# Performance work log

Measured on AMD Instinct MI355X. Metric: run time of the kernel, lower is better.

## Reference

```python
import jax, jax.numpy as jnp
import numpy as np

N, E, G, L, H, DIN = 50000, 800000, 500, 4, 64, 128
EPS = 1e-5


def _gcn(x, W, b, src, dst, n):
    h = x @ W
    loop = jnp.arange(n)
    s = jnp.concatenate([src, loop])
    d = jnp.concatenate([dst, loop])
    deg = jax.ops.segment_sum(jnp.ones(s.shape[0], x.dtype), d, num_segments=n)
    dinv = jax.lax.rsqrt(jnp.maximum(deg, 1.0))  # deg >= 1 due to self loops
    norm = (dinv[s] * dinv[d])[:, None]
    return jax.ops.segment_sum(h[s] * norm, d, num_segments=n) + b


def _g2(x, W, b, src, dst, n, p=2.0):
    # G2 gradient gate: tau = tanh(scatter_mean_over_src(|X_src - X_dst|^p))
    Xc = jax.nn.relu(_gcn(x, W, b, src, dst, n))
    diff = jnp.abs(Xc[src] - Xc[dst]) ** p  # [E, H]
    s = jax.ops.segment_sum(diff, src, num_segments=n)
    cnt = jax.ops.segment_sum(jnp.ones(src.shape[0], x.dtype), src, num_segments=n)
    return jnp.tanh(s / jnp.maximum(cnt, 1.0)[:, None])


def _bn(x, g, b):
    # BatchNorm1d with batch statistics (training-mode normalization)
    m = x.mean(0)
    v = x.var(0)
    return (x - m) * jax.lax.rsqrt(v + EPS) * g + b


def setup_inputs() -> dict:
    key = jax.random.key(0)
    ks = jax.random.split(key, 24)
    sc_in = 1.0 / np.sqrt(DIN)
    sc_h = 1.0 / np.sqrt(H)
    inp = {
        "x": jax.random.normal(ks[0], (N, DIN), jnp.float32),
        "edge_index": jax.random.randint(ks[1], (2, E), 0, N),
        "batch": jnp.sort(jax.random.randint(ks[2], (N,), 0, G)),
        "preW": jax.random.normal(ks[3], (DIN, H), jnp.float32) * sc_in,
        "preb": jnp.zeros((H,), jnp.float32),
        "convW": jax.random.normal(ks[4], (L, H, H), jnp.float32) * sc_h,
        "convb": jnp.zeros((L, H), jnp.float32),
        "ggW": jax.random.normal(ks[5], (L, H, H), jnp.float32) * sc_h,
        "ggb": jnp.zeros((L, H), jnp.float32),
        "lin1W": jax.random.normal(ks[6], (H, H), jnp.float32) * sc_h,
        "lin1b": jnp.zeros((H,), jnp.float32),
        "lin2W": jax.random.normal(ks[7], (H, H), jnp.float32) * sc_h,
        "lin2b": jnp.zeros((H,), jnp.float32),
        "lin3W": jax.random.normal(ks[8], (H, H), jnp.float32) * sc_h,
        "lin3b": jnp.zeros((H,), jnp.float32),
        "lin4W": jax.random.normal(ks[9], (H, 1), jnp.float32) * sc_h,
        "lin4b": jnp.zeros((1,), jnp.float32),
        "bn_g": jnp.ones((H,), jnp.float32),
        "bn_b": jnp.zeros((H,), jnp.float32),
    }
    return inp


def reference(x, edge_index, batch, preW, preb, convW, convb, ggW, ggb,
              lin1W, lin1b, lin2W, lin2b, lin3W, lin3b, lin4W, lin4b,
              bn_g, bn_b):
    src, dst = edge_index[0], edge_index[1]
    # prelinear (dropout disabled / eval)
    x = jax.nn.relu(x @ preW + preb)
    for l in range(L):
        x_ = jax.nn.relu(_gcn(x, convW[l], convb[l], src, dst, N))
        tau = _g2(x, ggW[l], ggb[l], src, dst, N)
        x = (1.0 - tau) * x + tau * x_
    # readout: global add pool per graph -> [G, H]
    h = jax.ops.segment_sum(x, batch, num_segments=G)
    out = jax.nn.relu(_bn(h @ lin1W + lin1b, bn_g, bn_b))
    out = jax.nn.relu(_bn(out @ lin2W + lin2b, bn_g, bn_b))
    out = jax.nn.relu(_bn(out @ lin3W + lin3b, bn_g, bn_b))
    out = out @ lin4W + lin4b  # [G, 1]
    energy = 0.5 * jnp.sum((x[src] - x[dst]) ** 2)  # dirichlet energy of final x
    return (out, out, energy)
```

## Files before the change

kernel.cpp:

```cpp
#include <hip/hip_runtime.h>
#include <hip/hip_bf16.h>


#define N_NODES 50000
#define N_EDGES 800000
#define N_GRAPH 500
#define N_LAYERS 4
#define HDIM 64
#define DDIN 128
#define BN_EPS 1e-5f
#define NEPART 256


__global__ __launch_bounds__(256) void k_degrees(const int* __restrict__ ei,
                                                 int* __restrict__ deg_in,
                                                 int* __restrict__ deg_out) {
  int e = blockIdx.x * 256 + threadIdx.x;
  if (e >= N_EDGES) return;
  int s = ei[e], d = ei[N_EDGES + e];
  atomicAdd(&deg_out[s], 1);
  atomicAdd(&deg_in[d], 1);
}

__global__ __launch_bounds__(1024) void k_scan(const int* __restrict__ a0, int* __restrict__ o0,
                                               int* __restrict__ c0,
                                               const int* __restrict__ a1, int* __restrict__ o1,
                                               int* __restrict__ c1) {
  __shared__ int sh[1024];
  const int T = 1024, C = 8;
  for (int pass = 0; pass < 2; ++pass) {
    const int* in = pass ? a1 : a0;
    int* out = pass ? o1 : o0;
    int* cur = pass ? c1 : c0;
    int carry = 0;
    for (int base = 0; base < N_NODES; base += T * C) {
      int idx0 = base + threadIdx.x * C;
      int v[C];
      int s = 0;
#pragma unroll
      for (int j = 0; j < C; ++j) {
        int ii = idx0 + j;
        v[j] = (ii < N_NODES) ? in[ii] : 0;
        s += v[j];
      }
      sh[threadIdx.x] = s;
      __syncthreads();
      for (int off = 1; off < T; off <<= 1) {
        int t = (threadIdx.x >= off) ? sh[threadIdx.x - off] : 0;
        __syncthreads();
        if (threadIdx.x >= off) sh[threadIdx.x] += t;
        __syncthreads();
      }
      int incl = sh[threadIdx.x];
      int excl = incl - s;
      int run = carry + excl;
#pragma unroll
      for (int j = 0; j < C; ++j) {
        int ii = idx0 + j;
        if (ii < N_NODES) {
          out[ii] = run;
          cur[ii] = run;
        }
        run += v[j];
      }
      int total = sh[T - 1];
      __syncthreads();
      carry += total;
    }
    if (threadIdx.x == 0) out[N_NODES] = carry;
    __syncthreads();
  }
}

__global__ __launch_bounds__(256) void k_fill(const int* __restrict__ ei,
                                              int* __restrict__ cur_dst,
                                              int* __restrict__ cur_src,
                                              int* __restrict__ csr_dst,
                                              int* __restrict__ csr_src) {
  int e = blockIdx.x * 256 + threadIdx.x;
  if (e >= N_EDGES) return;
  int s = ei[e], d = ei[N_EDGES + e];
  int p = atomicAdd(&cur_dst[d], 1);
  csr_dst[p] = s;
  int q = atomicAdd(&cur_src[s], 1);
  csr_src[q] = d;
}

__global__ __launch_bounds__(256) void k_dinv(const int* __restrict__ deg_in,
                                              float* __restrict__ dinv) {
  int i = blockIdx.x * 256 + threadIdx.x;
  if (i >= N_NODES) return;
  dinv[i] = rsqrtf((float)(deg_in[i] + 1));
}


__global__ __launch_bounds__(256) void k_prelin(const float* __restrict__ x0,
                                                const float* __restrict__ W,
                                                const float* __restrict__ b,
                                                float* __restrict__ x) {
  __shared__ float Ws[DDIN * HDIM];
  for (int t = threadIdx.x; t < DDIN * HDIM; t += 256) Ws[t] = W[t];
  __syncthreads();
  int wave = threadIdx.x >> 6, lane = threadIdx.x & 63;
  float bias = b[lane];
  int stride = gridDim.x * 4;
  for (int i = blockIdx.x * 4 + wave; i < N_NODES; i += stride) {
    const float* xr = x0 + (size_t)i * DDIN;
    float xl0 = xr[lane], xl1 = xr[64 + lane];
    float acc = bias;
#pragma unroll
    for (int k = 0; k < 64; ++k) acc = fmaf(__shfl(xl0, k), Ws[k * 64 + lane], acc);
#pragma unroll
    for (int k = 0; k < 64; ++k) acc = fmaf(__shfl(xl1, k), Ws[(64 + k) * 64 + lane], acc);
    x[(size_t)i * HDIM + lane] = fmaxf(acc, 0.f);
  }
}

__global__ __launch_bounds__(256) void k_gemm2(const float* __restrict__ agg,
                                               const float* __restrict__ W1,
                                               const float* __restrict__ W2,
                                               const float* __restrict__ b1,
                                               const float* __restrict__ b2,
                                               float* __restrict__ x_,
                                               float* __restrict__ Xc) {
  __shared__ float W1s[HDIM * HDIM], W2s[HDIM * HDIM];
  for (int t = threadIdx.x; t < HDIM * HDIM; t += 256) {
    W1s[t] = W1[t];
    W2s[t] = W2[t];
  }
  __syncthreads();
  int wave = threadIdx.x >> 6, lane = threadIdx.x & 63;
  float bb1 = b1[lane], bb2 = b2[lane];
  int stride = gridDim.x * 4;
  for (int i = blockIdx.x * 4 + wave; i < N_NODES; i += stride) {
    float xl = agg[(size_t)i * HDIM + lane];
    float a1 = 0.f, a2 = 0.f;
#pragma unroll
    for (int k = 0; k < 64; ++k) {
      float xv = __shfl(xl, k);
      a1 = fmaf(xv, W1s[k * 64 + lane], a1);
      a2 = fmaf(xv, W2s[k * 64 + lane], a2);
    }
    x_[(size_t)i * HDIM + lane] = fmaxf(a1 + bb1, 0.f);
    Xc[(size_t)i * HDIM + lane] = fmaxf(a2 + bb2, 0.f);
  }
}


__global__ __launch_bounds__(256) void k_agg(const float* __restrict__ x,
                                             const int* __restrict__ rp,
                                             const int* __restrict__ csr,
                                             const float* __restrict__ dinv,
                                             float* __restrict__ agg) {
  int i = (blockIdx.x * 256 + threadIdx.x) >> 6;
  int lane = threadIdx.x & 63;
  if (i >= N_NODES) return;
  int e0 = rp[i], e1 = rp[i + 1];
  float di = dinv[i];
  size_t li = (size_t)i * HDIM + lane;
  float a0 = x[li] * di, a1 = 0.f, a2 = 0.f, a3 = 0.f;
  for (int base = e0; base < e1; base += 64) {
    int m = e1 - base;
    if (m > 64) m = 64;
    int idx = csr[base + (lane < m ? lane : 0)];
    float dv = dinv[idx];
    int k = 0;
    for (; k + 8 <= m; k += 8) {
      int s0 = __shfl(idx, k), s1 = __shfl(idx, k + 1), s2 = __shfl(idx, k + 2),
          s3 = __shfl(idx, k + 3), s4 = __shfl(idx, k + 4), s5 = __shfl(idx, k + 5),
          s6 = __shfl(idx, k + 6), s7 = __shfl(idx, k + 7);
      float w0 = __shfl(dv, k), w1 = __shfl(dv, k + 1), w2 = __shfl(dv, k + 2),
            w3 = __shfl(dv, k + 3), w4 = __shfl(dv, k + 4), w5 = __shfl(dv, k + 5),
            w6 = __shfl(dv, k + 6), w7 = __shfl(dv, k + 7);
      float v0 = x[(size_t)s0 * HDIM + lane], v1 = x[(size_t)s1 * HDIM + lane];
      float v2 = x[(size_t)s2 * HDIM + lane], v3 = x[(size_t)s3 * HDIM + lane];
      float v4 = x[(size_t)s4 * HDIM + lane], v5 = x[(size_t)s5 * HDIM + lane];
      float v6 = x[(size_t)s6 * HDIM + lane], v7 = x[(size_t)s7 * HDIM + lane];
      a0 = fmaf(v0, w0, a0);
      a1 = fmaf(v1, w1, a1);
      a2 = fmaf(v2, w2, a2);
      a3 = fmaf(v3, w3, a3);
      a0 = fmaf(v4, w4, a0);
      a1 = fmaf(v5, w5, a1);
      a2 = fmaf(v6, w6, a2);
      a3 = fmaf(v7, w7, a3);
    }
    for (; k < m; ++k) {
      int s = __shfl(idx, k);
      float w = __shfl(dv, k);
      a0 = fmaf(x[(size_t)s * HDIM + lane], w, a0);
    }
  }
  agg[li] = (a0 + a1 + a2 + a3) * di;
}

__global__ __launch_bounds__(256) void k_gate(const float* __restrict__ Xc,
                                              const float* __restrict__ x_,
                                              const int* __restrict__ rp,
                                              const int* __restrict__ csr,
                                              float* __restrict__ x) {
  int i = (blockIdx.x * 256 + threadIdx.x) >> 6;
  int lane = threadIdx.x & 63;
  if (i >= N_NODES) return;
  int e0 = rp[i], e1 = rp[i + 1];
  float xi = Xc[(size_t)i * HDIM + lane];
  float a0 = 0.f, a1 = 0.f, a2 = 0.f, a3 = 0.f;
  for (int base = e0; base < e1; base += 64) {
    int m = e1 - base;
    if (m > 64) m = 64;
    int idx = csr[base + (lane < m ? lane : 0)];
    int k = 0;
    for (; k + 8 <= m; k += 8) {
      int s0 = __shfl(idx, k), s1 = __shfl(idx, k + 1), s2 = __shfl(idx, k + 2),
          s3 = __shfl(idx, k + 3), s4 = __shfl(idx, k + 4), s5 = __shfl(idx, k + 5),
          s6 = __shfl(idx, k + 6), s7 = __shfl(idx, k + 7);
      float v0 = Xc[(size_t)s0 * HDIM + lane], v1 = Xc[(size_t)s1 * HDIM + lane];
      float v2 = Xc[(size_t)s2 * HDIM + lane], v3 = Xc[(size_t)s3 * HDIM + lane];
      float v4 = Xc[(size_t)s4 * HDIM + lane], v5 = Xc[(size_t)s5 * HDIM + lane];
      float v6 = Xc[(size_t)s6 * HDIM + lane], v7 = Xc[(size_t)s7 * HDIM + lane];
      float t0 = xi - v0, t1 = xi - v1, t2 = xi - v2, t3 = xi - v3;
      float t4 = xi - v4, t5 = xi - v5, t6 = xi - v6, t7 = xi - v7;
      a0 = fmaf(t0, t0, a0);
      a1 = fmaf(t1, t1, a1);
      a2 = fmaf(t2, t2, a2);
      a3 = fmaf(t3, t3, a3);
      a0 = fmaf(t4, t4, a0);
      a1 = fmaf(t5, t5, a1);
      a2 = fmaf(t6, t6, a2);
      a3 = fmaf(t7, t7, a3);
    }
    for (; k < m; ++k) {
      int d = __shfl(idx, k);
      float t = xi - Xc[(size_t)d * HDIM + lane];
      a0 = fmaf(t, t, a0);
    }
  }
  int cnt = e1 - e0;
  float tau = tanhf((a0 + a1 + a2 + a3) / (float)(cnt > 0 ? cnt : 1));
  size_t idx = (size_t)i * HDIM + lane;
  x[idx] = (1.f - tau) * x[idx] + tau * x_[idx];
}

__global__ __launch_bounds__(256) void k_epool(const float* __restrict__ x,
                                               const int* __restrict__ rp,
                                               const int* __restrict__ csr,
                                               const int* __restrict__ batch,
                                               float* __restrict__ hpool,
                                               float* __restrict__ epart) {
  int i = (blockIdx.x * 256 + threadIdx.x) >> 6;
  int lane = threadIdx.x & 63;
  if (i >= N_NODES) return;
  float xi = x[(size_t)i * HDIM + lane];
  int e0 = rp[i], e1 = rp[i + 1];
  float a0 = 0.f, a1 = 0.f, a2 = 0.f, a3 = 0.f;
  for (int base = e0; base < e1; base += 64) {
    int m = e1 - base;
    if (m > 64) m = 64;
    int idx = csr[base + (lane < m ? lane : 0)];
    int k = 0;
    for (; k + 8 <= m; k += 8) {
      int s0 = __shfl(idx, k), s1 = __shfl(idx, k + 1), s2 = __shfl(idx, k + 2),
          s3 = __shfl(idx, k + 3), s4 = __shfl(idx, k + 4), s5 = __shfl(idx, k + 5),
          s6 = __shfl(idx, k + 6), s7 = __shfl(idx, k + 7);
      float v0 = x[(size_t)s0 * HDIM + lane], v1 = x[(size_t)s1 * HDIM + lane];
      float v2 = x[(size_t)s2 * HDIM + lane], v3 = x[(size_t)s3 * HDIM + lane];
      float v4 = x[(size_t)s4 * HDIM + lane], v5 = x[(size_t)s5 * HDIM + lane];
      float v6 = x[(size_t)s6 * HDIM + lane], v7 = x[(size_t)s7 * HDIM + lane];
      float t0 = xi - v0, t1 = xi - v1, t2 = xi - v2, t3 = xi - v3;
      float t4 = xi - v4, t5 = xi - v5, t6 = xi - v6, t7 = xi - v7;
      a0 = fmaf(t0, t0, a0);
      a1 = fmaf(t1, t1, a1);
      a2 = fmaf(t2, t2, a2);
      a3 = fmaf(t3, t3, a3);
      a0 = fmaf(t4, t4, a0);
      a1 = fmaf(t5, t5, a1);
      a2 = fmaf(t6, t6, a2);
      a3 = fmaf(t7, t7, a3);
    }
    for (; k < m; ++k) {
      int d = __shfl(idx, k);
      float t = xi - x[(size_t)d * HDIM + lane];
      a0 = fmaf(t, t, a0);
    }
  }
  int g = batch[i];
  atomicAdd(&hpool[g * HDIM + lane], xi);
  float acc = a0 + a1 + a2 + a3;
  acc += __shfl_down(acc, 32);
  acc += __shfl_down(acc, 16);
  acc += __shfl_down(acc, 8);
  acc += __shfl_down(acc, 4);
  acc += __shfl_down(acc, 2);
  acc += __shfl_down(acc, 1);
  if (lane == 0) atomicAdd(&epart[i & (NEPART - 1)], acc);
}

__global__ __launch_bounds__(256) void k_esum(const float* __restrict__ epart,
                                              float* __restrict__ out_e) {
  __shared__ float sh[NEPART];
  int t = threadIdx.x;
  sh[t] = epart[t];
  __syncthreads();
  for (int off = NEPART / 2; off > 0; off >>= 1) {
    if (t < off) sh[t] += sh[t + off];
    __syncthreads();
  }
  if (t == 0) out_e[0] = 0.5f * sh[0];
}


__global__ __launch_bounds__(64) void k_mlp(const float* __restrict__ Hin,
                                            const float* __restrict__ W,
                                            const float* __restrict__ b,
                                            float* __restrict__ Z) {
  int r = blockIdx.x, c = threadIdx.x;
  float xl = Hin[r * HDIM + c];
  float acc = b[c];
#pragma unroll
  for (int k = 0; k < 64; ++k) acc = fmaf(__shfl(xl, k), W[k * HDIM + c], acc);
  Z[r * HDIM + c] = acc;
}

__global__ __launch_bounds__(256) void k_bn(float* __restrict__ Z,
                                            const float* __restrict__ g,
                                            const float* __restrict__ b) {
  int c = blockIdx.x;
  int tid = threadIdx.x;
  __shared__ float red[256];
  float v0 = (tid < N_GRAPH) ? Z[tid * HDIM + c] : 0.f;
  float v1 = (tid + 256 < N_GRAPH) ? Z[(tid + 256) * HDIM + c] : 0.f;
  red[tid] = v0 + v1;
  __syncthreads();
  for (int off = 128; off > 0; off >>= 1) {
    if (tid < off) red[tid] += red[tid + off];
    __syncthreads();
  }
  float mean = red[0] / (float)N_GRAPH;
  __syncthreads();
  float d0 = (tid < N_GRAPH) ? v0 - mean : 0.f;
  float d1 = (tid + 256 < N_GRAPH) ? v1 - mean : 0.f;
  red[tid] = d0 * d0 + d1 * d1;
  __syncthreads();
  for (int off = 128; off > 0; off >>= 1) {
    if (tid < off) red[tid] += red[tid + off];
    __syncthreads();
  }
  float var = red[0] / (float)N_GRAPH;
  float scale = rsqrtf(var + BN_EPS) * g[c];
  float bias = b[c];
  if (tid < N_GRAPH) Z[tid * HDIM + c] = fmaxf(fmaf(d0, scale, bias), 0.f);
  if (tid + 256 < N_GRAPH) Z[(tid + 256) * HDIM + c] = fmaxf(fmaf(d1, scale, bias), 0.f);
}

__global__ __launch_bounds__(256) void k_final(const float* __restrict__ H,
                                               const float* __restrict__ w,
                                               const float* __restrict__ b,
                                               float* __restrict__ out) {
  int r = blockIdx.x * 256 + threadIdx.x;
  if (r >= N_GRAPH) return;
  float acc = b[0];
#pragma unroll
  for (int k = 0; k < 64; ++k) acc = fmaf(H[r * HDIM + k], w[k], acc);
  out[r] = acc;
  out[N_GRAPH + r] = acc;
}


extern "C" void kernel_launch(void* const* d_in, const int* in_sizes, int n_in,
                              void* d_out, int out_size, void* d_ws, size_t ws_size,
                              hipStream_t stream) {
  (void)in_sizes; (void)n_in; (void)out_size; (void)ws_size;
  const float* x0    = (const float*)d_in[0];
  const int*   ei    = (const int*)d_in[1];
  const int*   batch = (const int*)d_in[2];
  const float* preW  = (const float*)d_in[3];
  const float* preb  = (const float*)d_in[4];
  const float* convW = (const float*)d_in[5];
  const float* convb = (const float*)d_in[6];
  const float* ggW   = (const float*)d_in[7];
  const float* ggb   = (const float*)d_in[8];
  const float* lin1W = (const float*)d_in[9];
  const float* lin1b = (const float*)d_in[10];
  const float* lin2W = (const float*)d_in[11];
  const float* lin2b = (const float*)d_in[12];
  const float* lin3W = (const float*)d_in[13];
  const float* lin3b = (const float*)d_in[14];
  const float* lin4W = (const float*)d_in[15];
  const float* lin4b = (const float*)d_in[16];
  const float* bng   = (const float*)d_in[17];
  const float* bnb   = (const float*)d_in[18];
  float* out = (float*)d_out;

  char* ws = (char*)d_ws;
  size_t off = 0;
  auto alloc = [&](size_t bytes) -> void* {
    off = (off + 255) & ~(size_t)255;
    void* p = ws + off;
    off += bytes;
    return p;
  };
  int* deg_in   = (int*)alloc(2ull * N_NODES * 4);
  int* deg_out  = deg_in + N_NODES;
  int* rp_dst   = (int*)alloc((N_NODES + 1) * 4);
  int* rp_src   = (int*)alloc((N_NODES + 1) * 4);
  int* cur_dst  = (int*)alloc((N_NODES + 1) * 4);
  int* cur_src  = (int*)alloc((N_NODES + 1) * 4);
  int* csr_dst  = (int*)alloc((size_t)N_EDGES * 4);
  int* csr_src  = (int*)alloc((size_t)N_EDGES * 4);
  float* dinv   = (float*)alloc(N_NODES * 4);
  float* x      = (float*)alloc((size_t)N_NODES * HDIM * 4);
  float* aggb   = (float*)alloc((size_t)N_NODES * HDIM * 4);
  float* x_     = (float*)alloc((size_t)N_NODES * HDIM * 4);
  float* Xc     = (float*)alloc((size_t)N_NODES * HDIM * 4);
  float* hpool  = (float*)alloc(N_GRAPH * HDIM * 4);
  float* epart  = (float*)alloc(NEPART * 4);
  float* mlpA   = (float*)alloc(N_GRAPH * HDIM * 4);
  float* mlpB   = (float*)alloc(N_GRAPH * HDIM * 4);

  hipMemsetAsync(deg_in, 0, 2ull * N_NODES * 4, stream);
  hipMemsetAsync(hpool, 0, N_GRAPH * HDIM * 4, stream);
  hipMemsetAsync(epart, 0, NEPART * 4, stream);

  k_degrees<<<(N_EDGES + 255) / 256, 256, 0, stream>>>(ei, deg_in, deg_out);
  k_scan<<<1, 1024, 0, stream>>>(deg_in, rp_dst, cur_dst, deg_out, rp_src, cur_src);
  k_fill<<<(N_EDGES + 255) / 256, 256, 0, stream>>>(ei, cur_dst, cur_src, csr_dst, csr_src);
  k_dinv<<<(N_NODES + 255) / 256, 256, 0, stream>>>(deg_in, dinv);

  k_prelin<<<512, 256, 0, stream>>>(x0, preW, preb, x);

  const int gnode = (N_NODES + 3) / 4;
  for (int l = 0; l < N_LAYERS; ++l) {
    k_agg<<<gnode, 256, 0, stream>>>(x, rp_dst, csr_dst, dinv, aggb);
    k_gemm2<<<1024, 256, 0, stream>>>(aggb, convW + l * HDIM * HDIM, ggW + l * HDIM * HDIM,
                                      convb + l * HDIM, ggb + l * HDIM, x_, Xc);
    k_gate<<<gnode, 256, 0, stream>>>(Xc, x_, rp_src, csr_src, x);
  }

  k_epool<<<gnode, 256, 0, stream>>>(x, rp_src, csr_src, batch, hpool, epart);
  k_esum<<<1, NEPART, 0, stream>>>(epart, out + 2 * N_GRAPH);

  k_mlp<<<N_GRAPH, 64, 0, stream>>>(hpool, lin1W, lin1b, mlpA);
  k_bn<<<HDIM, 256, 0, stream>>>(mlpA, bng, bnb);
  k_mlp<<<N_GRAPH, 64, 0, stream>>>(mlpA, lin2W, lin2b, mlpB);
  k_bn<<<HDIM, 256, 0, stream>>>(mlpB, bng, bnb);
  k_mlp<<<N_GRAPH, 64, 0, stream>>>(mlpB, lin3W, lin3b, mlpA);
  k_bn<<<HDIM, 256, 0, stream>>>(mlpA, bng, bnb);
  k_final<<<(N_GRAPH + 255) / 256, 256, 0, stream>>>(mlpA, lin4W, lin4b, out);
}
```

Before: 1.073 ms.

## Parallelize CSR prefix scan across blocks and fuse aggregation into dual GEMM

Replaces the single-block serial scan with a three-phase multi-block scan (block scans, block-offset scan, offset add) that also computes dinv, removing one launch. Fuses the GCN neighbor aggregation into the dual 64x64 GEMM kernel so the aggregated features stay in registers instead of round-tripping through a global buffer each layer. The fused kernel uses a persistent grid of 1024 blocks with 32KB shared memory for weights, which may lower occupancy and latency hiding for the gather-heavy aggregation.

```diff
diff --git a/kernel.cpp b/kernel.cpp
--- a/kernel.cpp
+++ b/kernel.cpp
@@ -10,6 +10,8 @@
 #define DDIN 128
 #define BN_EPS 1e-5f
 #define NEPART 256
+#define SC_CHUNK 2048
+#define SC_NBLK ((N_NODES + SC_CHUNK - 1) / SC_CHUNK)
 
 
 __global__ __launch_bounds__(256) void k_degrees(const int* __restrict__ ei,
@@ -22,53 +24,83 @@
   atomicAdd(&deg_in[d], 1);
 }
 
-__global__ __launch_bounds__(1024) void k_scan(const int* __restrict__ a0, int* __restrict__ o0,
-                                               int* __restrict__ c0,
-                                               const int* __restrict__ a1, int* __restrict__ o1,
-                                               int* __restrict__ c1) {
-  __shared__ int sh[1024];
-  const int T = 1024, C = 8;
-  for (int pass = 0; pass < 2; ++pass) {
-    const int* in = pass ? a1 : a0;
-    int* out = pass ? o1 : o0;
-    int* cur = pass ? c1 : c0;
-    int carry = 0;
-    for (int base = 0; base < N_NODES; base += T * C) {
-      int idx0 = base + threadIdx.x * C;
-      int v[C];
-      int s = 0;
-#pragma unroll
-      for (int j = 0; j < C; ++j) {
-        int ii = idx0 + j;
-        v[j] = (ii < N_NODES) ? in[ii] : 0;
-        s += v[j];
-      }
-      sh[threadIdx.x] = s;
-      __syncthreads();
-      for (int off = 1; off < T; off <<= 1) {
-        int t = (threadIdx.x >= off) ? sh[threadIdx.x - off] : 0;
-        __syncthreads();
-        if (threadIdx.x >= off) sh[threadIdx.x] += t;
-        __syncthreads();
-      }
-      int incl = sh[threadIdx.x];
-      int excl = incl - s;
-      int run = carry + excl;
-#pragma unroll
-      for (int j = 0; j < C; ++j) {
-        int ii = idx0 + j;
-        if (ii < N_NODES) {
-          out[ii] = run;
-          cur[ii] = run;
-        }
-        run += v[j];
-      }
-      int total = sh[T - 1];
-      __syncthreads();
-      carry += total;
-    }
-    if (threadIdx.x == 0) out[N_NODES] = carry;
+__global__ __launch_bounds__(256) void k_scan1(const int* __restrict__ deg_in,
+                                               const int* __restrict__ deg_out,
+                                               int* __restrict__ rp_dst,
+                                               int* __restrict__ rp_src,
+                                               int* __restrict__ bsum) {
+  int arr = blockIdx.y;
+  const int* in = arr ? deg_out : deg_in;
+  int* out = arr ? rp_src : rp_dst;
+  int base = blockIdx.x * SC_CHUNK + threadIdx.x * 8;
+  int v[8];
+  int s = 0;
+#pragma unroll
+  for (int j = 0; j < 8; ++j) {
+    int ii = base + j;
+    v[j] = (ii < N_NODES) ? in[ii] : 0;
+    s += v[j];
+  }
+  __shared__ int sh[256];
+  sh[threadIdx.x] = s;
+  __syncthreads();
+  for (int off = 1; off < 256; off <<= 1) {
+    int t = (threadIdx.x >= off) ? sh[threadIdx.x - off] : 0;
     __syncthreads();
+    sh[threadIdx.x] += t;
+    __syncthreads();
+  }
+  int run = sh[threadIdx.x] - s;
+#pragma unroll
+  for (int j = 0; j < 8; ++j) {
+    int ii = base + j;
+    if (ii < N_NODES) out[ii] = run;
+    run += v[j];
+  }
+  if (threadIdx.x == 255) bsum[arr * SC_NBLK + blockIdx.x] = sh[255];
+}
+
+__global__ __launch_bounds__(64) void k_scan2(const int* __restrict__ bsum,
+                                              int* __restrict__ boff,
+                                              int* __restrict__ rp_dst,
+                                              int* __restrict__ rp_src) {
+  int lane = threadIdx.x;
+  for (int a = 0; a < 2; ++a) {
+    int v = (lane < SC_NBLK) ? bsum[a * SC_NBLK + lane] : 0;
+    int incl = v;
+    for (int off = 1; off < 64; off <<= 1) {
+      int t = __shfl_up(incl, off);
+      if (lane >= off) incl += t;
+    }
+    if (lane < SC_NBLK) boff[a * SC_NBLK + lane] = incl - v;
+  }
+  if (lane == 0) {
+    rp_dst[N_NODES] = N_EDGES;
+    rp_src[N_NODES] = N_EDGES;
+  }
+}
+
+__global__ __launch_bounds__(256) void k_scan3(const int* __restrict__ boff,
+                                               int* __restrict__ rp_dst,
+                                               int* __restrict__ rp_src,
+                                               int* __restrict__ cur_dst,
+                                               int* __restrict__ cur_src,
+                                               const int* __restrict__ deg_in,
+                                               float* __restrict__ dinv) {
+  int arr = blockIdx.y;
+  int* rp = arr ? rp_src : rp_dst;
+  int* cur = arr ? cur_src : cur_dst;
+  int off = boff[arr * SC_NBLK + blockIdx.x];
+  int base = blockIdx.x * SC_CHUNK + threadIdx.x * 8;
+#pragma unroll
+  for (int j = 0; j < 8; ++j) {
+    int ii = base + j;
+    if (ii < N_NODES) {
+      int v = rp[ii] + off;
+      rp[ii] = v;
+      cur[ii] = v;
+      if (arr == 0) dinv[ii] = rsqrtf((float)(deg_in[ii] + 1));
+    }
   }
 }
 
@@ -86,13 +118,6 @@
   csr_src[q] = d;
 }
 
-__global__ __launch_bounds__(256) void k_dinv(const int* __restrict__ deg_in,
-                                              float* __restrict__ dinv) {
-  int i = blockIdx.x * 256 + threadIdx.x;
-  if (i >= N_NODES) return;
-  dinv[i] = rsqrtf((float)(deg_in[i] + 1));
-}
-
 
 __global__ __launch_bounds__(256) void k_prelin(const float* __restrict__ x0,
                                                 const float* __restrict__ W,
@@ -116,13 +141,16 @@
   }
 }
 
-__global__ __launch_bounds__(256) void k_gemm2(const float* __restrict__ agg,
-                                               const float* __restrict__ W1,
-                                               const float* __restrict__ W2,
-                                               const float* __restrict__ b1,
-                                               const float* __restrict__ b2,
-                                               float* __restrict__ x_,
-                                               float* __restrict__ Xc) {
+__global__ __launch_bounds__(256) void k_agg_gemm(const float* __restrict__ x,
+                                                  const int* __restrict__ rp,
+                                                  const int* __restrict__ csr,
+                                                  const float* __restrict__ dinv,
+                                                  const float* __restrict__ W1,
+                                                  const float* __restrict__ W2,
+                                                  const float* __restrict__ b1,
+                                                  const float* __restrict__ b2,
+                                                  float* __restrict__ x_,
+                                                  float* __restrict__ Xc) {
   __shared__ float W1s[HDIM * HDIM], W2s[HDIM * HDIM];
   for (int t = threadIdx.x; t < HDIM * HDIM; t += 256) {
     W1s[t] = W1[t];
@@ -133,65 +161,53 @@
   float bb1 = b1[lane], bb2 = b2[lane];
   int stride = gridDim.x * 4;
   for (int i = blockIdx.x * 4 + wave; i < N_NODES; i += stride) {
-    float xl = agg[(size_t)i * HDIM + lane];
-    float a1 = 0.f, a2 = 0.f;
+    int e0 = rp[i], e1 = rp[i + 1];
+    float di = dinv[i];
+    size_t li = (size_t)i * HDIM + lane;
+    float a0 = x[li] * di, a1 = 0.f, a2 = 0.f, a3 = 0.f;
+    for (int base = e0; base < e1; base += 64) {
+      int m = e1 - base;
+      if (m > 64) m = 64;
+      int idx = csr[base + (lane < m ? lane : 0)];
+      float dv = dinv[idx];
+      int k = 0;
+      for (; k + 8 <= m; k += 8) {
+        int s0 = __shfl(idx, k), s1 = __shfl(idx, k + 1), s2 = __shfl(idx, k + 2),
+            s3 = __shfl(idx, k + 3), s4 = __shfl(idx, k + 4), s5 = __shfl(idx, k + 5),
+            s6 = __shfl(idx, k + 6), s7 = __shfl(idx, k + 7);
+        float w0 = __shfl(dv, k), w1 = __shfl(dv, k + 1), w2 = __shfl(dv, k + 2),
+              w3 = __shfl(dv, k + 3), w4 = __shfl(dv, k + 4), w5 = __shfl(dv, k + 5),
+              w6 = __shfl(dv, k + 6), w7 = __shfl(dv, k + 7);
+        float v0 = x[(size_t)s0 * HDIM + lane], v1 = x[(size_t)s1 * HDIM + lane];
+        float v2 = x[(size_t)s2 * HDIM + lane], v3 = x[(size_t)s3 * HDIM + lane];
+        float v4 = x[(size_t)s4 * HDIM + lane], v5 = x[(size_t)s5 * HDIM + lane];
+        float v6 = x[(size_t)s6 * HDIM + lane], v7 = x[(size_t)s7 * HDIM + lane];
+        a0 = fmaf(v0, w0, a0);
+        a1 = fmaf(v1, w1, a1);
+        a2 = fmaf(v2, w2, a2);
+        a3 = fmaf(v3, w3, a3);
+        a0 = fmaf(v4, w4, a0);
+        a1 = fmaf(v5, w5, a1);
+        a2 = fmaf(v6, w6, a2);
+        a3 = fmaf(v7, w7, a3);
+      }
+      for (; k < m; ++k) {
+        int s = __shfl(idx, k);
+        float w = __shfl(dv, k);
+        a0 = fmaf(x[(size_t)s * HDIM + lane], w, a0);
+      }
+    }
+    float acc = (a0 + a1 + a2 + a3) * di;
+    float r1 = 0.f, r2 = 0.f;
 #pragma unroll
     for (int k = 0; k < 64; ++k) {
-      float xv = __shfl(xl, k);
-      a1 = fmaf(xv, W1s[k * 64 + lane], a1);
-      a2 = fmaf(xv, W2s[k * 64 + lane], a2);
-    }
-    x_[(size_t)i * HDIM + lane] = fmaxf(a1 + bb1, 0.f);
-    Xc[(size_t)i * HDIM + lane] = fmaxf(a2 + bb2, 0.f);
-  }
-}
-
-
-__global__ __launch_bounds__(256) void k_agg(const float* __restrict__ x,
-                                             const int* __restrict__ rp,
-                                             const int* __restrict__ csr,
-                                             const float* __restrict__ dinv,
-                                             float* __restrict__ agg) {
-  int i = (blockIdx.x * 256 + threadIdx.x) >> 6;
-  int lane = threadIdx.x & 63;
-  if (i >= N_NODES) return;
-  int e0 = rp[i], e1 = rp[i + 1];
-  float di = dinv[i];
-  size_t li = (size_t)i * HDIM + lane;
-  float a0 = x[li] * di, a1 = 0.f, a2 = 0.f, a3 = 0.f;
-  for (int base = e0; base < e1; base += 64) {
-    int m = e1 - base;
-    if (m > 64) m = 64;
-    int idx = csr[base + (lane < m ? lane : 0)];
-    float dv = dinv[idx];
-    int k = 0;
-    for (; k + 8 <= m; k += 8) {
-      int s0 = __shfl(idx, k), s1 = __shfl(idx, k + 1), s2 = __shfl(idx, k + 2),
-          s3 = __shfl(idx, k + 3), s4 = __shfl(idx, k + 4), s5 = __shfl(idx, k + 5),
-          s6 = __shfl(idx, k + 6), s7 = __shfl(idx, k + 7);
-      float w0 = __shfl(dv, k), w1 = __shfl(dv, k + 1), w2 = __shfl(dv, k + 2),
-            w3 = __shfl(dv, k + 3), w4 = __shfl(dv, k + 4), w5 = __shfl(dv, k + 5),
-            w6 = __shfl(dv, k + 6), w7 = __shfl(dv, k + 7);
-      float v0 = x[(size_t)s0 * HDIM + lane], v1 = x[(size_t)s1 * HDIM + lane];
-      float v2 = x[(size_t)s2 * HDIM + lane], v3 = x[(size_t)s3 * HDIM + lane];
-      float v4 = x[(size_t)s4 * HDIM + lane], v5 = x[(size_t)s5 * HDIM + lane];
-      float v6 = x[(size_t)s6 * HDIM + lane], v7 = x[(size_t)s7 * HDIM + lane];
-      a0 = fmaf(v0, w0, a0);
-      a1 = fmaf(v1, w1, a1);
-      a2 = fmaf(v2, w2, a2);
-      a3 = fmaf(v3, w3, a3);
-      a0 = fmaf(v4, w4, a0);
-      a1 = fmaf(v5, w5, a1);
-      a2 = fmaf(v6, w6, a2);
-      a3 = fmaf(v7, w7, a3);
-    }
-    for (; k < m; ++k) {
-      int s = __shfl(idx, k);
-      float w = __shfl(dv, k);
-      a0 = fmaf(x[(size_t)s * HDIM + lane], w, a0);
-    }
-  }
-  agg[li] = (a0 + a1 + a2 + a3) * di;
+      float xv = __shfl(acc, k);
+      r1 = fmaf(xv, W1s[k * 64 + lane], r1);
+      r2 = fmaf(xv, W2s[k * 64 + lane], r2);
+    }
+    x_[li] = fmaxf(r1 + bb1, 0.f);
+    Xc[li] = fmaxf(r2 + bb2, 0.f);
+  }
 }
 
 __global__ __launch_bounds__(256) void k_gate(const float* __restrict__ Xc,
@@ -405,11 +421,12 @@
   int* rp_src   = (int*)alloc((N_NODES + 1) * 4);
   int* cur_dst  = (int*)alloc((N_NODES + 1) * 4);
   int* cur_src  = (int*)alloc((N_NODES + 1) * 4);
+  int* bsum     = (int*)alloc(2 * SC_NBLK * 4);
+  int* boff     = (int*)alloc(2 * SC_NBLK * 4);
   int* csr_dst  = (int*)alloc((size_t)N_EDGES * 4);
   int* csr_src  = (int*)alloc((size_t)N_EDGES * 4);
   float* dinv   = (float*)alloc(N_NODES * 4);
   float* x      = (float*)alloc((size_t)N_NODES * HDIM * 4);
-  float* aggb   = (float*)alloc((size_t)N_NODES * HDIM * 4);
   float* x_     = (float*)alloc((size_t)N_NODES * HDIM * 4);
   float* Xc     = (float*)alloc((size_t)N_NODES * HDIM * 4);
   float* hpool  = (float*)alloc(N_GRAPH * HDIM * 4);
@@ -422,17 +439,21 @@
   hipMemsetAsync(epart, 0, NEPART * 4, stream);
 
   k_degrees<<<(N_EDGES + 255) / 256, 256, 0, stream>>>(ei, deg_in, deg_out);
-  k_scan<<<1, 1024, 0, stream>>>(deg_in, rp_dst, cur_dst, deg_out, rp_src, cur_src);
+  {
+    dim3 g(SC_NBLK, 2);
+    k_scan1<<<g, 256, 0, stream>>>(deg_in, deg_out, rp_dst, rp_src, bsum);
+    k_scan2<<<1, 64, 0, stream>>>(bsum, boff, rp_dst, rp_src);
+    k_scan3<<<g, 256, 0, stream>>>(boff, rp_dst, rp_src, cur_dst, cur_src, deg_in, dinv);
+  }
   k_fill<<<(N_EDGES + 255) / 256, 256, 0, stream>>>(ei, cur_dst, cur_src, csr_dst, csr_src);
-  k_dinv<<<(N_NODES + 255) / 256, 256, 0, stream>>>(deg_in, dinv);
 
   k_prelin<<<512, 256, 0, stream>>>(x0, preW, preb, x);
 
   const int gnode = (N_NODES + 3) / 4;
   for (int l = 0; l < N_LAYERS; ++l) {
-    k_agg<<<gnode, 256, 0, stream>>>(x, rp_dst, csr_dst, dinv, aggb);
-    k_gemm2<<<1024, 256, 0, stream>>>(aggb, convW + l * HDIM * HDIM, ggW + l * HDIM * HDIM,
-                                      convb + l * HDIM, ggb + l * HDIM, x_, Xc);
+    k_agg_gemm<<<1024, 256, 0, stream>>>(x, rp_dst, csr_dst, dinv,
+                                         convW + l * HDIM * HDIM, ggW + l * HDIM * HDIM,
+                                         convb + l * HDIM, ggb + l * HDIM, x_, Xc);
     k_gate<<<gnode, 256, 0, stream>>>(Xc, x_, rp_src, csr_src, x);
   }
 
```

Result: faster. 1.024 ms (-4.5%).
